# Kernel optimization log

Hardware: AMD Instinct MI355X
Metric: run time of the kernel (lower is better)

The kernel has to match this reference:

```python
import jax, jax.numpy as jnp
import numpy as np

N_NODES, LATENT_DIM = 16, 8
BOX = 10.0                      # periodic box size (minimum-image convention)
BATCH = 32768
N_POLY, N_SELECT = 1000, 512
SOFT = 1e-3                     # softening constant
POWERS = (2, 3, 4, 5, 6, 8, 10, 12, 14)

# static index sets (constants, match torch.triu_indices offset=1 ordering)
IU, JU = np.triu_indices(N_NODES, k=1)      # node pairs, P = 120
II, JJ = np.triu_indices(LATENT_DIM, k=1)   # intra-latent dim pairs, 28


def setup_inputs() -> dict:
    key = jax.random.key(0)
    k1, k2, k3, k4 = jax.random.split(key, 4)
    D = N_NODES * LATENT_DIM
    return {
        "z_flat": jax.random.normal(k1, (BATCH, D), jnp.float32),
        "z_mean": jax.random.normal(k2, (D,), jnp.float32),
        "z_std": jnp.ones((D,), jnp.float32),
        "x_poly_mean": jax.random.normal(k3, (N_POLY,), jnp.float32),
        "x_poly_std": jnp.ones((N_POLY,), jnp.float32),
        "feature_mask": jax.random.randint(k4, (N_SELECT,), 0, N_POLY, jnp.int32),
    }


def reference(z_flat, z_mean, z_std, x_poly_mean, x_poly_std, feature_mask):
    z = jnp.clip(z_flat, -1e6, 1e6)
    B = z.shape[0]
    zn = (z - z_mean) / z_std                       # normalized raw latents [B, 128]
    nodes = z.reshape(B, N_NODES, LATENT_DIM)

    # --- pairwise distance features on first 2 latent dims, minimum image ---
    diff = nodes[:, IU, :2] - nodes[:, JU, :2]      # [B, P, 2]
    diff = diff - BOX * jnp.round(diff / BOX)
    d = jnp.sqrt(jnp.sum(diff * diff, axis=2)) + 1e-6   # [B, P]
    e = jnp.exp(-d)
    dist = [d, 1.0 / (d + SOFT)]
    dist += [1.0 / (d ** n + SOFT) for n in POWERS]
    dist += [e, e / (d + SOFT), jnp.log(d + SOFT)]

    X = jnp.clip(jnp.concatenate([zn] + dist, axis=1), -1e6, 1e6)   # [B, 1808]

    # --- physics-informed expansion ---
    Xn = zn.reshape(B, N_NODES, LATENT_DIM)
    p_sq = jnp.sum(Xn[:, :, LATENT_DIM // 2:] ** 2, axis=2)         # [B, 16]
    intra = (Xn[:, :, II] * Xn[:, :, JJ]).reshape(B, -1)            # [B, 16*28]
    inter = (Xn[:, IU, :] * Xn[:, JU, :]).reshape(B, -1)            # [B, 120*8]
    Xe = jnp.concatenate([
        X, zn ** 2, jnp.sin(zn), jnp.cos(zn),
        jnp.log(jnp.abs(zn) + 1e-3), jnp.exp(jnp.clip(zn, -10, 2)),
        p_sq, intra, inter,
    ], axis=1)                                                       # [B, 3872]

    # variance-based top-1000 selection (unbiased variance, as torch.var)
    if Xe.shape[1] > N_POLY:
        var = jnp.var(Xe, axis=0, ddof=1)
        _, top = jax.lax.top_k(var, N_POLY)
        Xe = Xe[:, top]

    Xe = jnp.clip(jnp.nan_to_num(Xe, nan=0.0, posinf=1e9, neginf=-1e9), -1e12, 1e12)

    # masked selection + normalization
    sel = Xe[:, feature_mask]
    return (sel - x_poly_mean[feature_mask]) / x_poly_std[feature_mask]
```

## Files before the change

kernel.cpp:

```cpp
#include <hip/hip_runtime.h>
#include <cstdint>
#include <cstddef>

#define NFEAT 3872
#define NPAIR 120
#define NB    32768
#define ZD    128
#define NPOLY 1000
#define NSEL  512
#define SOFT  1e-3f

#define STHREADS 512
#define NZSLOT   1856
#define ZCHUNK   4
#define SB       64
#define RO       8
#define VCHUNK   32
#define RSLICE   32
#define RGSZ     121
#define MAXT     1280


__device__ __forceinline__ float frcp(float x) {
  float r = __builtin_amdgcn_rcpf(x);
  float e = fmaf(-x, r, 1.0f);
  return fmaf(r, e, r);
}
__device__ __forceinline__ float frcpr(float x) {
  return __builtin_amdgcn_rcpf(x);
}

#define FSIN(x) __sinf(x)
#define FCOS(x) __cosf(x)
#define FLOG(x) __logf(x)
#define FEXP(x) __expf(x)

__device__ __forceinline__ void init_tables_par(int tid, unsigned char* IUs, unsigned char* JUs,
                                                unsigned char* IIs, unsigned char* JJs) {
  if (tid < NPAIR) {
    int i = 0, rem = tid;
    while (rem >= 15 - i) { rem -= 15 - i; ++i; }
    IUs[tid] = (unsigned char)i; JUs[tid] = (unsigned char)(i + 1 + rem);
  }
  if (tid < 28) {
    int i = 0, rem = tid;
    while (rem >= 7 - i) { rem -= 7 - i; ++i; }
    IIs[tid] = (unsigned char)i; JJs[tid] = (unsigned char)(i + 1 + rem);
  }
}

__device__ __forceinline__ int pack_plan(int f, const unsigned char* IUs, const unsigned char* JUs,
                                         const unsigned char* IIs, const unsigned char* JJs) {
  int op = 31, a0 = 0, a1 = 0;
  if (f < 128) { op = 0; a0 = f; }
  else if (f < 1808) {
    int t = f - 128; int b = t / 120; int p = t - b * 120; a0 = p;
    if (b == 0) op = 1;
    else if (b == 11) { op = 3; a1 = 0; }
    else if (b == 12) op = 4;
    else if (b == 13) { op = 5; a1 = 0; }
    else {
      const int P[10] = {1, 2, 3, 4, 5, 6, 8, 10, 12, 14};
      op = 2; a1 = P[b - 1];
    }
  }
  else if (f < 1936) { op = 8; a0 = f - 1808; a1 = a0; }
  else if (f < 2064) { op = 6; a0 = f - 1936; a1 = 0; }
  else if (f < 2192) { op = 6; a0 = f - 2064; a1 = 1; }
  else if (f < 2320) { op = 5; a0 = f - 2192; a1 = 1; }
  else if (f < 2448) { op = 3; a0 = f - 2320; a1 = 1; }
  else if (f < 2464) { op = 7; a0 = (f - 2448) * 8; }
  else if (f < 2912) { int t = f - 2464; int n = t / 28; int qq = t - n * 28;
                       op = 8; a0 = n * 8 + IIs[qq]; a1 = n * 8 + JJs[qq]; }
  else if (f < NFEAT) { int t = f - 2912; int p = t >> 3; int kk = t & 7;
                        op = 8; a0 = IUs[p] * 8 + kk; a1 = JUs[p] * 8 + kk; }
  return op | (a0 << 5) | (a1 << 12);
}

__device__ __forceinline__ int decode_zslot(int s, const unsigned char* IUs, const unsigned char* JUs,
                                            const unsigned char* IIs, const unsigned char* JJs) {
  int op = 0, a0 = 0, a1 = 0, fid = 4095;
  if (s < 128) { op = 1; a0 = s; fid = s; }
  else if (s < 256) { op = 2; a0 = s - 128; fid = 1936 + (s - 128); }
  else if (s < 384) { op = 3; a0 = s - 256; fid = 2192 + (s - 256); }
  else if (s < 448) {
    int q = s - 384;
    op = 4;
    a0 = (q < 16) ? q * 8 : 0;
    if (q < 16) fid = 2448 + q;
  } else if (s < 896) {
    int t = s - 448;
    int n = t / 28, qq = t - n * 28;
    op = 5; a0 = n * 8 + IIs[qq]; a1 = n * 8 + JJs[qq]; fid = 2464 + t;
  } else if (s < NZSLOT) {
    int t = s - 896;
    int p = t >> 3, kk = t & 7;
    op = 5; a0 = IUs[p] * 8 + kk; a1 = JUs[p] * 8 + kk; fid = 2912 + t;
  }
  return op | (a0 << 3) | (a1 << 10) | (fid << 17);
}

__global__ __launch_bounds__(STHREADS) void stats_kernel(const float* __restrict__ z,
                                                         const float* __restrict__ zmean,
                                                         const float* __restrict__ zstd,
                                                         float* __restrict__ psum,
                                                         float* __restrict__ psumsq,
                                                         int rows_per_block) {
  __shared__ __align__(16) union {
    struct { float zm[ZD]; float rz[ZD]; float zn[SB * ZD]; } zns;
    struct { float zc[SB * 32]; float red[4][2 * NPAIR]; } ds;
  } sh;
  __shared__ unsigned char IUs[NPAIR], JUs[NPAIR], IIs[28], JJs[28];
  int tid = threadIdx.x;
  init_tables_par(tid, IUs, JUs, IIs, JJs);
  int bx = blockIdx.x;
  int b = bx >> 1;
  int row0 = b * rows_per_block;
  int row1 = min(row0 + rows_per_block, NB);

  if ((bx & 1) == 0) {
    if (tid < ZD) { sh.zns.zm[tid] = zmean[tid]; sh.zns.rz[tid] = frcp(zstd[tid]); }
    __syncthreads();

    int plan[ZCHUNK];
#pragma unroll
    for (int k = 0; k < ZCHUNK; ++k)
      plan[k] = decode_zslot(tid + k * STHREADS, IUs, JUs, IIs, JJs);

    float s[ZCHUNK], q[ZCHUNK], s2 = 0.0f, q2 = 0.0f;
#pragma unroll
    for (int k = 0; k < ZCHUNK; ++k) { s[k] = 0.0f; q[k] = 0.0f; }

#define ROWLOOP _Pragma("unroll 8") for (int rr = 0; rr < SB; ++rr)
#define ACC  { sk += v; qk = fmaf(v, v, qk); }
#define ACC2 { sk2 += v2; qk2 = fmaf(v2, v2, qk2); }

    for (int r0 = row0; r0 < row1; r0 += SB) {
      const float4* z4 = (const float4*)(z + (size_t)r0 * ZD);
#pragma unroll
      for (int u = 0; u < SB * ZD / 4 / STHREADS; ++u) {
        int t = u * STHREADS + tid;
        float4 v = z4[t];
        int c4 = t & 31;
        v.x = fminf(fmaxf(v.x, -1e6f), 1e6f);
        v.y = fminf(fmaxf(v.y, -1e6f), 1e6f);
        v.z = fminf(fmaxf(v.z, -1e6f), 1e6f);
        v.w = fminf(fmaxf(v.w, -1e6f), 1e6f);
        float4 m4 = ((const float4*)sh.zns.zm)[c4];
        float4 r4 = ((const float4*)sh.zns.rz)[c4];
        float4 o;
        o.x = (v.x - m4.x) * r4.x;
        o.y = (v.y - m4.y) * r4.y;
        o.z = (v.z - m4.z) * r4.z;
        o.w = (v.w - m4.w) * r4.w;
        ((float4*)sh.zns.zn)[t] = o;
      }
      __syncthreads();
      const float* znS = sh.zns.zn;
      {
        int pk = plan[0];
        int a0 = (pk >> 3) & 127, a1 = (pk >> 10) & 127;
        int wop = __builtin_amdgcn_readfirstlane(pk & 7);
        float sk = 0.0f, qk = 0.0f, sk2 = 0.0f, qk2 = 0.0f;
        switch (wop) {
          case 1: ROWLOOP { float v = znS[rr * ZD + a0];
                            float v2 = v * v; ACC ACC2 } break;
          case 2: ROWLOOP { float x = znS[rr * ZD + a0];
                            float v, v2; __sincosf(x, &v, &v2); ACC ACC2 } break;
          case 3: ROWLOOP { float x = znS[rr * ZD + a0];
                            float v = FLOG(fabsf(x) + 0.001f);
                            float xc = fminf(fmaxf(x, -10.0f), 2.0f);
                            float v2 = FEXP(xc); ACC ACC2 } break;
          case 4: ROWLOOP { const float* zr = znS + rr * ZD + a0;
                            float x4 = zr[4]; float x5 = zr[5]; float x6 = zr[6]; float x7 = zr[7];
                            float v = x4 * x4 + x5 * x5 + x6 * x6 + x7 * x7; ACC } break;
          case 5: ROWLOOP { const float* zr = znS + rr * ZD; float v = zr[a0] * zr[a1]; ACC } break;
          default: break;
        }
        s[0] += sk; q[0] += qk;
        if (wop >= 1 && wop <= 3) { s2 += sk2; q2 += qk2; }
      }
#pragma unroll
      for (int k = 1; k < ZCHUNK; ++k) {
        int pk = plan[k];
        int a0 = (pk >> 3) & 127, a1 = (pk >> 10) & 127;
        int act = __builtin_amdgcn_readfirstlane((int)(((pk >> 17) & 4095) != 4095));
        if (act) {
          float sk = 0.0f, qk = 0.0f;
          ROWLOOP { const float* zr = znS + rr * ZD; float v = zr[a0] * zr[a1]; ACC }
          s[k] += sk; q[k] += qk;
        }
      }
      __syncthreads();
    }
#undef ROWLOOP
#undef ACC
#undef ACC2

#pragma unroll
    for (int k = 0; k < ZCHUNK; ++k) {
      int fid = (plan[k] >> 17) & 4095;
      int opk = plan[k] & 7;
      if (fid != 4095) {
        psum[(size_t)b * NFEAT + fid] = s[k];
        psumsq[(size_t)b * NFEAT + fid] = q[k];
        if (k == 0 && opk >= 1 && opk <= 3) {
          int fid2 = fid + ((opk == 1) ? 1808 : 128);
          psum[(size_t)b * NFEAT + fid2] = s2;
          psumsq[(size_t)b * NFEAT + fid2] = q2;
        }
      }
    }
  } else {
    __syncthreads();
    int p  = tid & 127;
    int rg = tid >> 7;
    int ni = (p < NPAIR) ? IUs[p] : 0;
    int nj = (p < NPAIR) ? JUs[p] : 0;

    float sF[14], qF[14];
#pragma unroll
    for (int bb = 0; bb < 14; ++bb) { sF[bb] = 0.0f; qF[bb] = 0.0f; }

    for (int r0 = row0; r0 < row1; r0 += SB) {
#pragma unroll
      for (int u = 0; u < SB * 32 / STHREADS; ++u) {
        int t = u * STHREADS + tid;
        int rr = t >> 5, c = t & 31;
        int col = ((c >> 1) << 3) + (c & 1);
        float v = z[(size_t)(r0 + rr) * ZD + col];
        sh.ds.zc[t] = fminf(fmaxf(v, -1e6f), 1e6f);
      }
      __syncthreads();
      if (p < NPAIR) {
        for (int rr = rg; rr < SB; rr += 4) {
          const float* zc = sh.ds.zc + rr * 32;
          float dx = zc[ni * 2 + 0] - zc[nj * 2 + 0];
          float dy = zc[ni * 2 + 1] - zc[nj * 2 + 1];
          dx = fmaf(-10.0f, rintf(dx * 0.1f), dx);
          dy = fmaf(-10.0f, rintf(dy * 0.1f), dy);
          float d = sqrtf(dx * dx + dy * dy) + 1e-6f;
          float e = FEXP(-d);
          float d2 = d * d,   d3 = d2 * d,  d4 = d2 * d2, d5 = d4 * d, d6 = d4 * d2;
          float d8 = d4 * d4, d10 = d8 * d2, d12 = d8 * d4, d14 = d12 * d2;
          float r1 = frcpr(d + SOFT);
          float v[14];
          v[0]  = d;
          v[1]  = r1;
          v[2]  = frcpr(d2 + SOFT);
          v[3]  = frcpr(d3 + SOFT);
          v[4]  = frcpr(d4 + SOFT);
          v[5]  = frcpr(d5 + SOFT);
          v[6]  = frcpr(d6 + SOFT);
          v[7]  = frcpr(d8 + SOFT);
          v[8]  = frcpr(d10 + SOFT);
          v[9]  = frcpr(d12 + SOFT);
          v[10] = frcpr(d14 + SOFT);
          v[11] = e;
          v[12] = e * r1;
          v[13] = FLOG(d + SOFT);
#pragma unroll
          for (int bb = 0; bb < 14; ++bb) {
            sF[bb] += v[bb];
            qF[bb] = fmaf(v[bb], v[bb], qF[bb]);
          }
        }
      }
      __syncthreads();
    }

    for (int bb = 0; bb < 14; ++bb) {
      if (p < NPAIR) {
        sh.ds.red[rg][p] = sF[bb];
        sh.ds.red[rg][NPAIR + p] = qF[bb];
      }
      __syncthreads();
      if (tid < 2 * NPAIR) {
        float t2 = ((sh.ds.red[0][tid] + sh.ds.red[1][tid]) + sh.ds.red[2][tid]) + sh.ds.red[3][tid];
        if (tid < NPAIR) psum[(size_t)b * NFEAT + 128 + bb * 120 + tid] = t2;
        else             psumsq[(size_t)b * NFEAT + 128 + bb * 120 + (tid - NPAIR)] = t2;
      }
      __syncthreads();
    }
  }
}

__global__ __launch_bounds__(256) void var1_kernel(const float* __restrict__ psum,
                                                   const float* __restrict__ psumsq,
                                                   double* __restrict__ psum2,
                                                   double* __restrict__ psumsq2,
                                                   int* __restrict__ rankA,
                                                   int slices) {
  int f = blockIdx.x * 256 + threadIdx.x;
  if (f >= NFEAT) return;
  if (blockIdx.y == 0) rankA[f] = 0;
  int b0 = blockIdx.y * slices;
  double s = 0.0, q = 0.0;
#pragma unroll 8
  for (int b = b0; b < b0 + slices; ++b) {
    s += (double)psum[(size_t)b * NFEAT + f];
    q += (double)psumsq[(size_t)b * NFEAT + f];
  }
  psum2[(size_t)blockIdx.y * NFEAT + f] = s;
  psumsq2[(size_t)blockIdx.y * NFEAT + f] = q;
}

__global__ __launch_bounds__(256) void var2rank1_kernel(const double* __restrict__ psum2,
                                                        const double* __restrict__ psumsq2,
                                                        int chunks,
                                                        int* __restrict__ rankA) {
  __shared__ double gvS[RGSZ];
  int tid = threadIdx.x;
  int g0 = blockIdx.y * RGSZ;
  const double N = (double)NB;
  if (tid < RGSZ) {
    double s = 0.0, q = 0.0;
#pragma unroll 8
    for (int b = 0; b < chunks; ++b) {
      s += psum2[(size_t)b * NFEAT + g0 + tid];
      q += psumsq2[(size_t)b * NFEAT + g0 + tid];
    }
    gvS[tid] = (q - s * s / N) / (N - 1.0);
  }
  __syncthreads();
  int f = blockIdx.x * 256 + tid;
  if (f >= NFEAT) return;
  double s = 0.0, q = 0.0;
#pragma unroll 8
  for (int b = 0; b < chunks; ++b) {
    s += psum2[(size_t)b * NFEAT + f];
    q += psumsq2[(size_t)b * NFEAT + f];
  }
  double vf = (q - s * s / N) / (N - 1.0);
  int cnt = 0;
#pragma unroll 11
  for (int k = 0; k < RGSZ; ++k) {
    double vg = gvS[k];
    int g = g0 + k;
    cnt += (int)((vg > vf) || (vg == vf && g < f));
  }
  atomicAdd(&rankA[f], cnt);
}

__global__ __launch_bounds__(1024) void rank2map_kernel(const int* __restrict__ rankA,
                                                        const int* __restrict__ mask,
                                                        const float* __restrict__ pmean,
                                                        const float* __restrict__ pstd,
                                                        int* __restrict__ taskW,
                                                        float* __restrict__ taskA,
                                                        float* __restrict__ taskB,
                                                        int* __restrict__ ntaskW) {
  __shared__ int topcolS[NPOLY];
  __shared__ int taskS[MAXT];
  __shared__ int cntS[32], pstartS[32];
  __shared__ int wcntS[8][32], wbaseS[8][32];
  __shared__ unsigned char IUs[NPAIR], JUs[NPAIR], IIs[28], JJs[28];
  int tid = threadIdx.x;
  init_tables_par(tid, IUs, JUs, IIs, JJs);
  for (int i = tid; i < MAXT; i += 1024) { taskS[i] = 31; taskA[i] = 0.0f; taskB[i] = 0.0f; }
  for (int f = tid; f < NFEAT; f += 1024) {
    int r = rankA[f];
    if (r < NPOLY) topcolS[r] = f;
  }
  __syncthreads();
  int pk = 31, op = 31;
  float aN = 0.0f, bN = 0.0f;
  int wave = tid >> 6, lane = tid & 63;
  unsigned long long mymask = 0;
  if (tid < NSEL) {
    int m = mask[tid];
    int c = topcolS[m];
    aN = frcp(pstd[m]);
    bN = -pmean[m] * aN;
    pk = pack_plan(c, IUs, JUs, IIs, JJs);
    op = pk & 31;
    for (int o = 0; o < 32; ++o) {
      unsigned long long bm = __ballot(op == o);
      if (lane == 0) wcntS[wave][o] = __popcll(bm);
      if (op == o) mymask = bm;
    }
  }
  __syncthreads();
  if (tid < 32) {
    int c = 0;
    for (int w2 = 0; w2 < 8; ++w2) { wbaseS[w2][tid] = c; c += wcntS[w2][tid]; }
    cntS[tid] = c;
  }
  __syncthreads();
  if (tid == 0) {
    int pcum = 0;
    for (int o = 0; o < 32; ++o) {
      pstartS[o] = pcum;
      pcum += (cntS[o] + 63) / 64 * 64;
    }
    ntaskW[0] = pcum;
  }
  __syncthreads();
  if (tid < NSEL) {
    int slot = pstartS[op] + wbaseS[wave][op]
             + (int)__popcll(mymask & ((1ull << lane) - 1ull));
    taskS[slot] = pk | (tid << 19);
    taskA[slot] = aN;
    taskB[slot] = bN;
  }
  __syncthreads();
  for (int i = tid; i < MAXT; i += 1024) taskW[i] = taskS[i];
}

__global__ __launch_bounds__(256, 6) void out_kernel(const float* __restrict__ z,
                                                     const float* __restrict__ zmean,
                                                     const float* __restrict__ zstd,
                                                     const int* __restrict__ taskW,
                                                     const float* __restrict__ taskA,
                                                     const float* __restrict__ taskB,
                                                     const int* __restrict__ ntaskW,
                                                     float* __restrict__ out,
                                                     int rows_per_block) {
  __shared__ __align__(16) float zmS[ZD];
  __shared__ __align__(16) float rzS[ZD];
  __shared__ __align__(16) float znS[RO * ZD];
  __shared__ float zcS[RO * 32], dS[RO * NPAIR];
  __shared__ __align__(16) float rowS[RO * NSEL];
  __shared__ unsigned char IUs[NPAIR], JUs[NPAIR], IIs[28], JJs[28];
  int tid = threadIdx.x;
  int row0 = blockIdx.x * rows_per_block;
  int row1 = min(row0 + rows_per_block, NB);
  const float4* z4 = (const float4*)(z + (size_t)row0 * ZD);
  float4 cur = z4[tid];
  init_tables_par(tid, IUs, JUs, IIs, JJs);
  if (tid < ZD) { zmS[tid] = zmean[tid]; rzS[tid] = frcp(zstd[tid]); }
  int ntask = ntaskW[0];
  __syncthreads();

  int nbat = (row1 - row0) / RO;
  for (int t2 = 0; t2 < nbat; ++t2) {
    int r0 = row0 + t2 * RO;
    {
      float4 v = cur;
      int rr = tid >> 5, c4 = tid & 31;
      v.x = fminf(fmaxf(v.x, -1e6f), 1e6f);
      v.y = fminf(fmaxf(v.y, -1e6f), 1e6f);
      v.z = fminf(fmaxf(v.z, -1e6f), 1e6f);
      v.w = fminf(fmaxf(v.w, -1e6f), 1e6f);
      if ((c4 & 1) == 0) {
        int node = c4 >> 1;
        zcS[rr * 32 + node * 2 + 0] = v.x;
        zcS[rr * 32 + node * 2 + 1] = v.y;
      }
      float4 m4 = ((const float4*)zmS)[c4];
      float4 s4 = ((const float4*)rzS)[c4];
      float4 o;
      o.x = (v.x - m4.x) * s4.x;
      o.y = (v.y - m4.y) * s4.y;
      o.z = (v.z - m4.z) * s4.z;
      o.w = (v.w - m4.w) * s4.w;
      ((float4*)znS)[tid] = o;
    }
    if (t2 + 1 < nbat) cur = z4[(size_t)(t2 + 1) * (RO * ZD / 4) + tid];
    __syncthreads();
    for (int t = tid; t < RO * 128; t += 256) {
      int p = t & 127;
      if (p < NPAIR) {
        int rr = t >> 7;
        int i = IUs[p], j = JUs[p];
        float dx = zcS[rr * 32 + i * 2 + 0] - zcS[rr * 32 + j * 2 + 0];
        float dy = zcS[rr * 32 + i * 2 + 1] - zcS[rr * 32 + j * 2 + 1];
        dx = fmaf(-10.0f, rintf(dx * 0.1f), dx);
        dy = fmaf(-10.0f, rintf(dy * 0.1f), dy);
        dS[rr * NPAIR + p] = sqrtf(dx * dx + dy * dy) + 1e-6f;
      }
    }
    __syncthreads();
#define RLV(BODY) { _Pragma("unroll") for (int rr = 0; rr < RO; ++rr) { \
      const float* znR = znS + rr * ZD; const float* dR = dS + rr * NPAIR; \
      (void)znR; (void)dR; float v; BODY; \
      if (valid) rowS[rr * NSEL + dst] = fmaf(v, aA, bA); } } break;
    {
      int s2 = tid;
      int pk = 31; float aA = 0.0f, bA = 0.0f;
      if (s2 < ntask) { pk = taskW[s2]; aA = taskA[s2]; bA = taskB[s2]; }
      for (; s2 < ntask; s2 += 256) {
        int s2n = s2 + 256;
        int pk_n = 31; float aA_n = 0.0f, bA_n = 0.0f;
        if (s2n < ntask) { pk_n = taskW[s2n]; aA_n = taskA[s2n]; bA_n = taskB[s2n]; }
        int op = pk & 31;
        int a0 = (pk >> 5) & 127, a1 = (pk >> 12) & 127, dst = (pk >> 19) & 511;
        bool valid = (op != 31);
        int wop = __builtin_amdgcn_readfirstlane(op);
        switch (wop) {
          case 0:  RLV({ v = znR[a0]; })
          case 1:  RLV({ v = dR[a0]; })
          case 2:  RLV({ float d = dR[a0];
                         float d2 = d * d;
                         float d4 = d2 * d2;
                         float d8 = d4 * d4;
                         float acc = (a1 & 8) ? d8 : 1.0f;
                         acc *= (a1 & 4) ? d4 : 1.0f;
                         acc *= (a1 & 2) ? d2 : 1.0f;
                         acc *= (a1 & 1) ? d  : 1.0f;
                         v = frcpr(acc + SOFT); })
          case 3:  RLV({ const float* src = a1 ? znR : dR;
                         float x = src[a0];
                         x = a1 ? fminf(fmaxf(x, -10.0f), 2.0f) : -x;
                         v = FEXP(x); })
          case 4:  RLV({ float d = dR[a0]; v = FEXP(-d) * frcpr(d + SOFT); })
          case 5:  RLV({ const float* src = a1 ? znR : dR;
                         float x = src[a0];
                         x = a1 ? fabsf(x) : x;
                         v = FLOG(x + SOFT); })
          case 6:  RLV({ float x = znR[a0];
                         float vs = FSIN(x);
                         float vc = FCOS(x);
                         v = a1 ? vc : vs; })
          case 7:  RLV({ const float* zr = znR + a0;
                         float x4 = zr[4]; float x5 = zr[5]; float x6 = zr[6]; float x7 = zr[7];
                         v = x4 * x4 + x5 * x5 + x6 * x6 + x7 * x7; })
          case 8:  RLV({ v = znR[a0] * znR[a1]; })
          default: break;
        }
        pk = pk_n; aA = aA_n; bA = bA_n;
      }
    }
#undef RLV
    __syncthreads();
    {
      float4* o4 = (float4*)(out + (size_t)r0 * NSEL);
      const float4* r4 = (const float4*)rowS;
      for (int t = tid; t < RO * NSEL / 4; t += 256) o4[t] = r4[t];
    }
    __syncthreads();
  }
}

extern "C" void kernel_launch(void* const* d_in, const int* in_sizes, int n_in,
                              void* d_out, int out_size, void* d_ws, size_t ws_size,
                              hipStream_t stream) {
  const float* z     = (const float*)d_in[0];
  const float* zmean = (const float*)d_in[1];
  const float* zstd  = (const float*)d_in[2];
  const float* pmean = (const float*)d_in[3];
  const float* pstd  = (const float*)d_in[4];
  const int*   mask  = (const int*)d_in[5];
  float* out = (float*)d_out;

  size_t tail = (size_t)VCHUNK * NFEAT * 16 + (size_t)NFEAT * 4
              + MAXT * 12 + 4096;
  int G = 512;
  while (G > 1 && (size_t)G * NFEAT * 8 + tail > ws_size) G >>= 1;
  int chunks = (G < VCHUNK) ? G : VCHUNK;
  int slices = G / chunks;

  char* w = (char*)d_ws;
  float*  psum    = (float*)w;                 w += (size_t)G * NFEAT * 4;
  float*  psumsq  = (float*)w;                 w += (size_t)G * NFEAT * 4;
  double* psum2   = (double*)w;                w += (size_t)VCHUNK * NFEAT * 8;
  double* psumsq2 = (double*)w;                w += (size_t)VCHUNK * NFEAT * 8;
  int*    rankA   = (int*)w;                   w += (size_t)NFEAT * 4;
  int*    taskW   = (int*)w;                   w += MAXT * 4;
  float*  taskA   = (float*)w;                 w += MAXT * 4;
  float*  taskB   = (float*)w;                 w += MAXT * 4;
  int*    ntaskW  = (int*)w;

  int rpb_stats = NB / G;
  stats_kernel<<<dim3(2 * G), dim3(STHREADS), 0, stream>>>(z, zmean, zstd, psum, psumsq,
                                                           rpb_stats);
  var1_kernel<<<dim3((NFEAT + 255) / 256, chunks), dim3(256), 0, stream>>>(psum, psumsq,
                                                                           psum2, psumsq2,
                                                                           rankA, slices);
  var2rank1_kernel<<<dim3((NFEAT + 255) / 256, RSLICE), dim3(256), 0, stream>>>(psum2, psumsq2,
                                                                                chunks, rankA);
  rank2map_kernel<<<dim3(1), dim3(1024), 0, stream>>>(rankA, mask, pmean, pstd,
                                                      taskW, taskA, taskB, ntaskW);
  const int rpb_out = 32;
  out_kernel<<<dim3(NB / rpb_out), dim3(256), 0, stream>>>(z, zmean, zstd, taskW, taskA, taskB,
                                                           ntaskW, out, rpb_out);
}
```

Measured before the change: 72.18 us.

## Fuse z-feature and distance-feature stats into one 1024-thread block per row group

Previously even and odd blocks split the work: one computed statistics for the z-derived features and the other for the pairwise distance features, and each loaded z separately. Now each 1024-thread block loads the z tile once, normalises it and writes the x/y columns to a second shared buffer, then computes both sets of statistics. Per-thread running sums for the z features are replaced by read-modify-write accumulation into global psum across row batches, and the final distance-feature reduction now combines eight row groups across four phases. This removes the duplicate global load of z and halves the block count, at the cost of more global stores per batch, larger blocks with higher register pressure under launch_bounds(1024, 8), and a longer serial instruction stream per block.

Result: slower. 83.39 us (+15.5%).

```diff
diff --git a/kernel.cpp b/kernel.cpp
--- a/kernel.cpp
+++ b/kernel.cpp
@@ -10,9 +10,9 @@
 #define NSEL  512
 #define SOFT  1e-3f
 
-#define STHREADS 512
+#define STHREADS 1024
 #define NZSLOT   1856
-#define ZCHUNK   4
+#define ZCHUNK   2
 #define SB       64
 #define RO       8
 #define VCHUNK   32
@@ -100,189 +100,183 @@
   return op | (a0 << 3) | (a1 << 10) | (fid << 17);
 }
 
-__global__ __launch_bounds__(STHREADS) void stats_kernel(const float* __restrict__ z,
-                                                         const float* __restrict__ zmean,
-                                                         const float* __restrict__ zstd,
-                                                         float* __restrict__ psum,
-                                                         float* __restrict__ psumsq,
-                                                         int rows_per_block) {
-  __shared__ __align__(16) union {
-    struct { float zm[ZD]; float rz[ZD]; float zn[SB * ZD]; } zns;
-    struct { float zc[SB * 32]; float red[4][2 * NPAIR]; } ds;
-  } sh;
+__global__ __launch_bounds__(STHREADS, 8) void stats_kernel(const float* __restrict__ z,
+                                                            const float* __restrict__ zmean,
+                                                            const float* __restrict__ zstd,
+                                                            float* __restrict__ psum,
+                                                            float* __restrict__ psumsq,
+                                                            int rows_per_block) {
+  __shared__ __align__(16) float zmS[ZD];
+  __shared__ __align__(16) float rzS[ZD];
+  __shared__ __align__(16) float zcS[SB * 32];
+  __shared__ __align__(16) float znOv[SB * ZD];
   __shared__ unsigned char IUs[NPAIR], JUs[NPAIR], IIs[28], JJs[28];
   int tid = threadIdx.x;
   init_tables_par(tid, IUs, JUs, IIs, JJs);
-  int bx = blockIdx.x;
-  int b = bx >> 1;
+  int b = blockIdx.x;
   int row0 = b * rows_per_block;
   int row1 = min(row0 + rows_per_block, NB);
-
-  if ((bx & 1) == 0) {
-    if (tid < ZD) { sh.zns.zm[tid] = zmean[tid]; sh.zns.rz[tid] = frcp(zstd[tid]); }
-    __syncthreads();
-
-    int plan[ZCHUNK];
+  if (tid < ZD) { zmS[tid] = zmean[tid]; rzS[tid] = frcp(zstd[tid]); }
+  __syncthreads();
+
+  int plan[ZCHUNK];
 #pragma unroll
-    for (int k = 0; k < ZCHUNK; ++k)
-      plan[k] = decode_zslot(tid + k * STHREADS, IUs, JUs, IIs, JJs);
-
-    float s[ZCHUNK], q[ZCHUNK], s2 = 0.0f, q2 = 0.0f;
+  for (int k = 0; k < ZCHUNK; ++k)
+    plan[k] = decode_zslot(tid + k * STHREADS, IUs, JUs, IIs, JJs);
+
+  int p  = tid & 127;
+  int rg = tid >> 7;
+  int ni = (p < NPAIR) ? IUs[p] : 0;
+  int nj = (p < NPAIR) ? JUs[p] : 0;
+
+  float sF[14], qF[14];
 #pragma unroll
-    for (int k = 0; k < ZCHUNK; ++k) { s[k] = 0.0f; q[k] = 0.0f; }
+  for (int bb = 0; bb < 14; ++bb) { sF[bb] = 0.0f; qF[bb] = 0.0f; }
+
+  size_t base = (size_t)b * NFEAT;
+  int nbat = (row1 - row0 + SB - 1) / SB;
 
 #define ROWLOOP _Pragma("unroll 8") for (int rr = 0; rr < SB; ++rr)
 #define ACC  { sk += v; qk = fmaf(v, v, qk); }
 #define ACC2 { sk2 += v2; qk2 = fmaf(v2, v2, qk2); }
-
-    for (int r0 = row0; r0 < row1; r0 += SB) {
+#define STOREACC(arr, idx, val) { if (tsb == 0) arr[idx] = (val); else arr[idx] += (val); }
+
+  for (int tsb = 0; tsb < nbat; ++tsb) {
+    int r0 = row0 + tsb * SB;
+    {
       const float4* z4 = (const float4*)(z + (size_t)r0 * ZD);
 #pragma unroll
       for (int u = 0; u < SB * ZD / 4 / STHREADS; ++u) {
         int t = u * STHREADS + tid;
         float4 v = z4[t];
         int c4 = t & 31;
+        int rr = t >> 5;
         v.x = fminf(fmaxf(v.x, -1e6f), 1e6f);
         v.y = fminf(fmaxf(v.y, -1e6f), 1e6f);
         v.z = fminf(fmaxf(v.z, -1e6f), 1e6f);
         v.w = fminf(fmaxf(v.w, -1e6f), 1e6f);
-        float4 m4 = ((const float4*)sh.zns.zm)[c4];
-        float4 r4 = ((const float4*)sh.zns.rz)[c4];
+        if ((c4 & 1) == 0) {
+          int node = c4 >> 1;
+          zcS[rr * 32 + node * 2 + 0] = v.x;
+          zcS[rr * 32 + node * 2 + 1] = v.y;
+        }
+        float4 m4 = ((const float4*)zmS)[c4];
+        float4 r4 = ((const float4*)rzS)[c4];
         float4 o;
         o.x = (v.x - m4.x) * r4.x;
         o.y = (v.y - m4.y) * r4.y;
         o.z = (v.z - m4.z) * r4.z;
         o.w = (v.w - m4.w) * r4.w;
-        ((float4*)sh.zns.zn)[t] = o;
-      }
-      __syncthreads();
-      const float* znS = sh.zns.zn;
-      {
-        int pk = plan[0];
-        int a0 = (pk >> 3) & 127, a1 = (pk >> 10) & 127;
-        int wop = __builtin_amdgcn_readfirstlane(pk & 7);
-        float sk = 0.0f, qk = 0.0f, sk2 = 0.0f, qk2 = 0.0f;
-        switch (wop) {
-          case 1: ROWLOOP { float v = znS[rr * ZD + a0];
-                            float v2 = v * v; ACC ACC2 } break;
-          case 2: ROWLOOP { float x = znS[rr * ZD + a0];
-                            float v, v2; __sincosf(x, &v, &v2); ACC ACC2 } break;
-          case 3: ROWLOOP { float x = znS[rr * ZD + a0];
-                            float v = FLOG(fabsf(x) + 0.001f);
-                            float xc = fminf(fmaxf(x, -10.0f), 2.0f);
-                            float v2 = FEXP(xc); ACC ACC2 } break;
-          case 4: ROWLOOP { const float* zr = znS + rr * ZD + a0;
-                            float x4 = zr[4]; float x5 = zr[5]; float x6 = zr[6]; float x7 = zr[7];
-                            float v = x4 * x4 + x5 * x5 + x6 * x6 + x7 * x7; ACC } break;
-          case 5: ROWLOOP { const float* zr = znS + rr * ZD; float v = zr[a0] * zr[a1]; ACC } break;
-          default: break;
+        ((float4*)znOv)[t] = o;
+      }
+    }
+    __syncthreads();
+    const float* znS = znOv;
+    {
+      int pk = plan[0];
+      int a0 = (pk >> 3) & 127, a1 = (pk >> 10) & 127;
+      int wop = __builtin_amdgcn_readfirstlane(pk & 7);
+      float sk = 0.0f, qk = 0.0f, sk2 = 0.0f, qk2 = 0.0f;
+      switch (wop) {
+        case 1: ROWLOOP { float v = znS[rr * ZD + a0];
+                          float v2 = v * v; ACC ACC2 } break;
+        case 2: ROWLOOP { float x = znS[rr * ZD + a0];
+                          float v, v2; __sincosf(x, &v, &v2); ACC ACC2 } break;
+        case 3: ROWLOOP { float x = znS[rr * ZD + a0];
+                          float v = FLOG(fabsf(x) + 0.001f);
+                          float xc = fminf(fmaxf(x, -10.0f), 2.0f);
+                          float v2 = FEXP(xc); ACC ACC2 } break;
+        case 4: ROWLOOP { const float* zr = znS + rr * ZD + a0;
+                          float x4 = zr[4]; float x5 = zr[5]; float x6 = zr[6]; float x7 = zr[7];
+                          float v = x4 * x4 + x5 * x5 + x6 * x6 + x7 * x7; ACC } break;
+        case 5: ROWLOOP { const float* zr = znS + rr * ZD; float v = zr[a0] * zr[a1]; ACC }
+                break;
+        default: break;
+      }
+      int fid = (pk >> 17) & 4095;
+      if (fid != 4095) {
+        STOREACC(psum, base + fid, sk)
+        STOREACC(psumsq, base + fid, qk)
+        if (wop >= 1 && wop <= 3) {
+          int fid2 = fid + ((wop == 1) ? 1808 : 128);
+          STOREACC(psum, base + fid2, sk2)
+          STOREACC(psumsq, base + fid2, qk2)
         }
-        s[0] += sk; q[0] += qk;
-        if (wop >= 1 && wop <= 3) { s2 += sk2; q2 += qk2; }
-      }
+      }
+    }
+    {
+      int pk = plan[1];
+      int a0 = (pk >> 3) & 127, a1 = (pk >> 10) & 127;
+      int fid = (pk >> 17) & 4095;
+      int act = __builtin_amdgcn_readfirstlane((int)(fid != 4095));
+      if (act) {
+        float sk = 0.0f, qk = 0.0f;
+        ROWLOOP { const float* zr = znS + rr * ZD; float v = zr[a0] * zr[a1]; ACC }
+        STOREACC(psum, base + fid, sk)
+        STOREACC(psumsq, base + fid, qk)
+      }
+    }
+    if (p < NPAIR) {
 #pragma unroll
-      for (int k = 1; k < ZCHUNK; ++k) {
-        int pk = plan[k];
-        int a0 = (pk >> 3) & 127, a1 = (pk >> 10) & 127;
-        int act = __builtin_amdgcn_readfirstlane((int)(((pk >> 17) & 4095) != 4095));
-        if (act) {
-          float sk = 0.0f, qk = 0.0f;
-          ROWLOOP { const float* zr = znS + rr * ZD; float v = zr[a0] * zr[a1]; ACC }
-          s[k] += sk; q[k] += qk;
+      for (int rx = 0; rx < 8; ++rx) {
+        const float* zc = zcS + (rg + rx * 8) * 32;
+        float dx = zc[ni * 2 + 0] - zc[nj * 2 + 0];
+        float dy = zc[ni * 2 + 1] - zc[nj * 2 + 1];
+        dx = fmaf(-10.0f, rintf(dx * 0.1f), dx);
+        dy = fmaf(-10.0f, rintf(dy * 0.1f), dy);
+        float d = sqrtf(dx * dx + dy * dy) + 1e-6f;
+        float e = FEXP(-d);
+        float d2 = d * d,   d3 = d2 * d,  d4 = d2 * d2, d5 = d4 * d, d6 = d4 * d2;
+        float d8 = d4 * d4, d10 = d8 * d2, d12 = d8 * d4, d14 = d12 * d2;
+        float r1 = frcpr(d + SOFT);
+        float v[14];
+        v[0]  = d;
+        v[1]  = r1;
+        v[2]  = frcpr(d2 + SOFT);
+        v[3]  = frcpr(d3 + SOFT);
+        v[4]  = frcpr(d4 + SOFT);
+        v[5]  = frcpr(d5 + SOFT);
+        v[6]  = frcpr(d6 + SOFT);
+        v[7]  = frcpr(d8 + SOFT);
+        v[8]  = frcpr(d10 + SOFT);
+        v[9]  = frcpr(d12 + SOFT);
+        v[10] = frcpr(d14 + SOFT);
+        v[11] = e;
+        v[12] = e * r1;
+        v[13] = FLOG(d + SOFT);
+#pragma unroll
+        for (int bb = 0; bb < 14; ++bb) {
+          sF[bb] += v[bb];
+          qF[bb] = fmaf(v[bb], v[bb], qF[bb]);
         }
       }
-      __syncthreads();
-    }
+    }
+    __syncthreads();
+  }
 #undef ROWLOOP
 #undef ACC
 #undef ACC2
-
-#pragma unroll
-    for (int k = 0; k < ZCHUNK; ++k) {
-      int fid = (plan[k] >> 17) & 4095;
-      int opk = plan[k] & 7;
-      if (fid != 4095) {
-        psum[(size_t)b * NFEAT + fid] = s[k];
-        psumsq[(size_t)b * NFEAT + fid] = q[k];
-        if (k == 0 && opk >= 1 && opk <= 3) {
-          int fid2 = fid + ((opk == 1) ? 1808 : 128);
-          psum[(size_t)b * NFEAT + fid2] = s2;
-          psumsq[(size_t)b * NFEAT + fid2] = q2;
-        }
-      }
-    }
-  } else {
-    __syncthreads();
-    int p  = tid & 127;
-    int rg = tid >> 7;
-    int ni = (p < NPAIR) ? IUs[p] : 0;
-    int nj = (p < NPAIR) ? JUs[p] : 0;
-
-    float sF[14], qF[14];
-#pragma unroll
-    for (int bb = 0; bb < 14; ++bb) { sF[bb] = 0.0f; qF[bb] = 0.0f; }
-
-    for (int r0 = row0; r0 < row1; r0 += SB) {
-#pragma unroll
-      for (int u = 0; u < SB * 32 / STHREADS; ++u) {
-        int t = u * STHREADS + tid;
-        int rr = t >> 5, c = t & 31;
-        int col = ((c >> 1) << 3) + (c & 1);
-        float v = z[(size_t)(r0 + rr) * ZD + col];
-        sh.ds.zc[t] = fminf(fmaxf(v, -1e6f), 1e6f);
-      }
-      __syncthreads();
-      if (p < NPAIR) {
-        for (int rr = rg; rr < SB; rr += 4) {
-          const float* zc = sh.ds.zc + rr * 32;
-          float dx = zc[ni * 2 + 0] - zc[nj * 2 + 0];
-          float dy = zc[ni * 2 + 1] - zc[nj * 2 + 1];
-          dx = fmaf(-10.0f, rintf(dx * 0.1f), dx);
-          dy = fmaf(-10.0f, rintf(dy * 0.1f), dy);
-          float d = sqrtf(dx * dx + dy * dy) + 1e-6f;
-          float e = FEXP(-d);
-          float d2 = d * d,   d3 = d2 * d,  d4 = d2 * d2, d5 = d4 * d, d6 = d4 * d2;
-          float d8 = d4 * d4, d10 = d8 * d2, d12 = d8 * d4, d14 = d12 * d2;
-          float r1 = frcpr(d + SOFT);
-          float v[14];
-          v[0]  = d;
-          v[1]  = r1;
-          v[2]  = frcpr(d2 + SOFT);
-          v[3]  = frcpr(d3 + SOFT);
-          v[4]  = frcpr(d4 + SOFT);
-          v[5]  = frcpr(d5 + SOFT);
-          v[6]  = frcpr(d6 + SOFT);
-          v[7]  = frcpr(d8 + SOFT);
-          v[8]  = frcpr(d10 + SOFT);
-          v[9]  = frcpr(d12 + SOFT);
-          v[10] = frcpr(d14 + SOFT);
-          v[11] = e;
-          v[12] = e * r1;
-          v[13] = FLOG(d + SOFT);
-#pragma unroll
-          for (int bb = 0; bb < 14; ++bb) {
-            sF[bb] += v[bb];
-            qF[bb] = fmaf(v[bb], v[bb], qF[bb]);
-          }
-        }
-      }
-      __syncthreads();
-    }
-
-    for (int bb = 0; bb < 14; ++bb) {
-      if (p < NPAIR) {
-        sh.ds.red[rg][p] = sF[bb];
-        sh.ds.red[rg][NPAIR + p] = qF[bb];
-      }
-      __syncthreads();
-      if (tid < 2 * NPAIR) {
-        float t2 = ((sh.ds.red[0][tid] + sh.ds.red[1][tid]) + sh.ds.red[2][tid]) + sh.ds.red[3][tid];
-        if (tid < NPAIR) psum[(size_t)b * NFEAT + 128 + bb * 120 + tid] = t2;
-        else             psumsq[(size_t)b * NFEAT + 128 + bb * 120 + (tid - NPAIR)] = t2;
-      }
-      __syncthreads();
-    }
-  }
+#undef STOREACC
+
+  float (*red)[7][NPAIR] = (float (*)[7][NPAIR])znOv;
+#define REDPHASE(SRC, OFF, DSTARR)                                            \
+  if (p < NPAIR) {                                                            \
+    _Pragma("unroll") for (int bb = 0; bb < 7; ++bb) red[rg][bb][p] = SRC[bb + OFF]; \
+  }                                                                           \
+  __syncthreads();                                                            \
+  for (int i = tid; i < 7 * NPAIR; i += STHREADS) {                           \
+    int bb = i / NPAIR, pp = i - bb * NPAIR;                                  \
+    float t2 = ((((((red[0][bb][pp] + red[1][bb][pp]) + red[2][bb][pp])       \
+               + red[3][bb][pp]) + red[4][bb][pp]) + red[5][bb][pp])          \
+               + red[6][bb][pp]) + red[7][bb][pp];                            \
+    DSTARR[base + 128 + (bb + OFF) * 120 + pp] = t2;                          \
+  }                                                                           \
+  __syncthreads();
+  REDPHASE(sF, 0, psum)
+  REDPHASE(sF, 7, psum)
+  REDPHASE(qF, 0, psumsq)
+  REDPHASE(qF, 7, psumsq)
+#undef REDPHASE
 }
 
 __global__ __launch_bounds__(256) void var1_kernel(const float* __restrict__ psum,
@@ -562,8 +556,8 @@
   int*    ntaskW  = (int*)w;
 
   int rpb_stats = NB / G;
-  stats_kernel<<<dim3(2 * G), dim3(STHREADS), 0, stream>>>(z, zmean, zstd, psum, psumsq,
-                                                           rpb_stats);
+  stats_kernel<<<dim3(G), dim3(STHREADS), 0, stream>>>(z, zmean, zstd, psum, psumsq,
+                                                       rpb_stats);
   var1_kernel<<<dim3((NFEAT + 255) / 256, chunks), dim3(256), 0, stream>>>(psum, psumsq,
                                                                            psum2, psumsq2,
                                                                            rankA, slices);
```
